# Optimization experiments

Measured on AMD Instinct MI355X. Metric: run time of the kernel, lower is better.

Reference implementation:

```python
import jax, jax.numpy as jnp
import numpy as np

B, IN, H = 256, 128, 512


def setup_inputs() -> dict:
    key = jax.random.key(0)
    ks = jax.random.split(key, 12)
    w = lambda k, shape: jax.random.normal(k, shape, dtype=jnp.float32) * 0.05
    return {
        "inputs": jax.random.normal(ks[0], (B, IN), dtype=jnp.float32),
        "h": jax.random.normal(ks[1], (B, H), dtype=jnp.float32),
        "c": jax.random.normal(ks[2], (B, H), dtype=jnp.float32),
        "ts": jax.random.uniform(ks[3], (B,), dtype=jnp.float32),
        # LSTMCell params (PyTorch layout: [4H, in], gate order i,f,g,o)
        "W_ih": w(ks[4], (4 * H, IN)),
        "W_hh": w(ks[5], (4 * H, H)),
        "b_ih": w(ks[6], (4 * H,)),
        "b_hh": w(ks[7], (4 * H,)),
        # ODE vector field: Linear(H,H) -> tanh -> Linear(H,H)
        "W1": w(ks[8], (H, H)),
        "b1": w(ks[9], (H,)),
        "W2": w(ks[10], (H, H)),
        "b2": w(ks[11], (H,)),
    }


def reference(inputs, h, c, ts, W_ih, W_hh, b_ih, b_hh, W1, b1, W2, b2):
    # --- LSTMCell ---
    gates = inputs @ W_ih.T + b_ih + h @ W_hh.T + b_hh  # [B, 4H]
    i_g, f_g, g_g, o_g = jnp.split(gates, 4, axis=-1)
    new_c = jax.nn.sigmoid(f_g) * c + jax.nn.sigmoid(i_g) * jnp.tanh(g_g)
    h0 = jax.nn.sigmoid(o_g) * jnp.tanh(new_c)  # [B, H]

    # --- sorted time grid ---
    bsz = ts.shape[0]
    indices = jnp.argsort(ts)
    s_sort = ts[indices] + jnp.linspace(0.0, 1e-4, bsz)  # strictly increasing

    # --- autonomous ODE vector field ---
    def f_ode(x):
        return jnp.tanh(x @ W1.T + b1) @ W2.T + b2

    # --- fixed-step RK4 trajectory at the sorted time points ---
    dts = s_sort[1:] - s_sort[:-1]  # [B-1]

    def step(hcur, dt):
        k1 = f_ode(hcur)
        k2 = f_ode(hcur + 0.5 * dt * k1)
        k3 = f_ode(hcur + 0.5 * dt * k2)
        k4 = f_ode(hcur + dt * k3)
        hn = hcur + (dt / 6.0) * (k1 + 2.0 * k2 + 2.0 * k3 + k4)
        return hn, hn

    _, traj_rest = jax.lax.scan(step, h0, dts)          # [B-1, B, H]
    traj = jnp.concatenate([h0[None], traj_rest], 0)    # [B, B, H]

    # per-batch-row time slice (faithful to trajectory[indices, arange(B)])
    new_h = traj[indices, jnp.arange(bsz)]  # [B, H]
    return new_h, new_c
```

## Files before the change

### kernel.cpp

```cpp
#include <hip/hip_runtime.h>

#define BB   256
#define IND  128
#define HD   512
#define KST  1
#define XSTR 648

typedef _Float16 f16x8 __attribute__((ext_vector_type(8)));
typedef float    f32x4 __attribute__((ext_vector_type(4)));

__device__ __forceinline__ float sigm(float x){ return 1.0f/(1.0f+__expf(-x)); }
__device__ __forceinline__ float tanhfast(float x){
  float e2 = __expf(2.0f*x);
  return 1.0f - 2.0f/(e2+1.0f);
}
__device__ __forceinline__ f16x8 cvt8(const float* s){
  f16x8 r;
  #pragma unroll
  for (int j=0;j<8;j++) r[j] = (_Float16)s[j];
  return r;
}

__device__ __forceinline__ f32x4 mv16(const _Float16* __restrict__ Ab,
    const f16x8* __restrict__ Bp, int m, int g){
  f16x8 af[16], bw[16];
  #pragma unroll
  for (int kt=0;kt<16;kt++)
    af[kt] = *(const f16x8*)&Ab[m*HD + kt*32 + 8*g];
  #pragma unroll
  for (int kt=0;kt<16;kt++)
    bw[kt] = Bp[kt*64];
  f32x4 acc = {0.f,0.f,0.f,0.f};
  #pragma unroll
  for (int kt=0;kt<16;kt++)
    acc = __builtin_amdgcn_mfma_f32_16x16x32_f16(af[kt], bw[kt], acc, 0,0,0);
  return acc;
}

__device__ __forceinline__ void packg_body(int b, int t,
    const float* __restrict__ Wih, const float* __restrict__ Whh,
    _Float16* __restrict__ Wgp){
  const int tile = b*4 + (t>>6);
  const int l = t & 63, m = l & 15, g = l >> 4;
  const int NT = tile/20, kt = tile - NT*20;
  const int n  = NT*16 + m;
  const int k0 = kt*32 + 8*g;
  const float* src = (kt < 4) ? (Wih + n*IND + k0) : (Whh + n*HD + (k0 - IND));
  *((f16x8*)(Wgp + tile*512) + l) = cvt8(src);
}

__device__ __forceinline__ void sort_body(int t, const float* __restrict__ ts,
    float* __restrict__ tau){
  __shared__ float sts[BB];
  __shared__ float ssort[BB];
  __shared__ int   sidx[BB];
  sts[t] = ts[t];
  __syncthreads();
  const float v = sts[t];
  int r = 0;
  for (int k=0;k<BB;k++){
    const float u = sts[k];
    r += (u < v) || (u == v && k < t);
  }
  ssort[r] = v + (float)r*(1e-4f/255.0f);
  sidx[r]  = t;
  __syncthreads();
  tau[t] = ssort[sidx[t]] - ssort[0];
}

__device__ __forceinline__ void packw_body(int tile, int t,
    const float* __restrict__ W, _Float16* __restrict__ Wp){
  const int l = t & 63, m = l & 15, g = l >> 4;
  const int NT = tile >> 4, kt = tile & 15;
  const float* src = W + (NT*16 + m)*HD + kt*32 + 8*g;
  *((f16x8*)(Wp + tile*512) + l) = cvt8(src);
}

__device__ __forceinline__ void packT_body(int unit, int t,
    const float* __restrict__ W2, _Float16* __restrict__ W2T){
  const int l = t & 63;
  const int kb = unit >> 5, jb = unit & 31;
  const int k0 = kb*64, j0 = jb*16;
  _Float16 v[16];
  #pragma unroll
  for (int i=0;i<16;i++)
    v[i] = (_Float16)W2[(j0+i)*HD + k0 + l];
  *(f16x8*)&W2T[(k0+l)*HD + j0]     = *(const f16x8*)&v[0];
  *(f16x8*)&W2T[(k0+l)*HD + j0 + 8] = *(const f16x8*)&v[8];
}

__device__ __forceinline__ void cvec_body(int n,
    const float* __restrict__ W1, const float* __restrict__ b2,
    float* __restrict__ cvec){
  float s = 0.f;
  for (int j=0;j<HD;j+=4){
    const float4 a = *(const float4*)(W1 + n*HD + j);
    const float4 bb = *(const float4*)(b2 + j);
    s += a.x*bb.x + a.y*bb.y + a.z*bb.z + a.w*bb.w;
  }
  cvec[n] = s;
}

__device__ __forceinline__ void gates_body(int b, int t,
    const float* __restrict__ inp, const float* __restrict__ h,
    const float* __restrict__ c,   const _Float16* __restrict__ Wgp,
    const float* __restrict__ bih, const float* __restrict__ bhh,
    _Float16* __restrict__ V, float* __restrict__ newc){
  __shared__ _Float16 X16[16*XSTR];
  __shared__ float    Gx[4][2][16][16];
  const int l = t & 63;
  const int w = t >> 6;
  const int m = l & 15;
  const int g = l >> 4;
  const int rt = b & 15;
  const int cq = b >> 4;
  const int r0 = rt * 16;

  for (int i=0;i<40;i++){
    const int e  = t + 256*i;
    const int rr = e / 640;
    const int k  = e - rr*640;
    const float v = (k < IND) ? inp[(r0+rr)*IND + k] : h[(r0+rr)*HD + (k-IND)];
    X16[rr*XSTR + k] = (_Float16)v;
  }
  __syncthreads();

  f16x8 af[20];
  #pragma unroll
  for (int kt=0;kt<20;kt++)
    af[kt] = *(const f16x8*)&X16[m*XSTR + kt*32 + 8*g];

  #pragma unroll
  for (int ht=0;ht<2;ht++){
    const int NT = w*32 + cq*2 + ht;
    const f16x8* bp = (const f16x8*)Wgp + (size_t)NT*20*64 + l;
    f16x8 bw[20];
    #pragma unroll
    for (int kt=0;kt<20;kt++) bw[kt] = bp[kt*64];
    f32x4 acc = {0.f,0.f,0.f,0.f};
    #pragma unroll
    for (int kt=0;kt<20;kt++)
      acc = __builtin_amdgcn_mfma_f32_16x16x32_f16(af[kt], bw[kt], acc, 0,0,0);
    #pragma unroll
    for (int r=0;r<4;r++) Gx[w][ht][4*g+r][m] = acc[r];
  }
  __syncthreads();

  #pragma unroll
  for (int p=0;p<2;p++){
    const int e   = t + 256*p;
    const int row = e >> 5;
    const int col = e & 31;
    const int ht  = col >> 4, mm = col & 15;
    const int hi  = cq*32 + col;
    const int grow = r0 + row;
    const float iv = Gx[0][ht][row][mm] + bih[hi]        + bhh[hi];
    const float fv = Gx[1][ht][row][mm] + bih[HD+hi]     + bhh[HD+hi];
    const float gv = Gx[2][ht][row][mm] + bih[2*HD+hi]   + bhh[2*HD+hi];
    const float ov = Gx[3][ht][row][mm] + bih[3*HD+hi]   + bhh[3*HD+hi];
    const float cv = c[grow*HD + hi];
    const float nc = sigm(fv)*cv + sigm(iv)*tanhfast(gv);
    const float hv = sigm(ov)*tanhfast(nc);
    newc[grow*HD + hi] = nc;
    V[grow*HD + hi]    = (_Float16)hv;
  }
}

__device__ __forceinline__ void mm_body(int tile, int t, int nw,
    const _Float16* __restrict__ W2T, const _Float16* __restrict__ W1p,
    _Float16* __restrict__ Mp){
  __shared__ float Mt[4][32][16];
  const int l = t & 63, w = t >> 6, m = l & 15, g = l >> 4;
  const int NT = tile >> 4, kt = tile & 15;
  const f16x8* bp = (const f16x8*)W1p + NT*16*64 + l;
  const f32x4 d0 = mv16(W2T + (kt*32     )*HD, bp, m, g);
  const f32x4 d1 = mv16(W2T + (kt*32 + 16)*HD, bp, m, g);
  #pragma unroll
  for (int r=0;r<4;r++){
    Mt[w][4*g+r][m]    = d0[r];
    Mt[w][16+4*g+r][m] = d1[r];
  }
  __syncthreads();
  _Float16 v[8];
  #pragma unroll
  for (int j=0;j<8;j++) v[j] = (_Float16)Mt[w][8*g+j][m];
  *((f16x8*)(Mp + tile*512) + l) = *(const f16x8*)v;
  (void)nw;
}

__device__ __forceinline__ void init0_body(int rb, int t,
    const _Float16* __restrict__ V, const _Float16* __restrict__ W1p,
    const float* __restrict__ b1, float* __restrict__ UB,
    _Float16* __restrict__ Y0, _Float16* __restrict__ YS0){
  const int l = t & 63, w = t >> 6, m = l & 15, g = l >> 4;
  const int rg = rb >> 4, cg = rb & 15;
  const int NT = cg*2 + w, cc = NT*16 + m;
  const f32x4 a = mv16(V + rg*16*HD, (const f16x8*)W1p + NT*16*64 + l, m, g);
  const float bv = b1[cc];
  #pragma unroll
  for (int r=0;r<4;r++){
    const int idx = (rg*16 + 4*g + r)*HD + cc;
    UB[idx] = a[r];
    const float y = tanhfast(a[r] + bv);
    Y0[idx]  = (_Float16)y;
    YS0[idx] = (_Float16)y;
  }
}


__global__ __launch_bounds__(256) void k_prep(
    const float* __restrict__ Wih, const float* __restrict__ Whh,
    const float* __restrict__ ts,  const float* __restrict__ W1,
    const float* __restrict__ W2,  const float* __restrict__ b2,
    _Float16* __restrict__ Wgp, float* __restrict__ tau,
    _Float16* __restrict__ W1p, _Float16* __restrict__ W2p,
    _Float16* __restrict__ W2T, float* __restrict__ cvec){
  const int b = blockIdx.x, t = threadIdx.x;
  if      (b < 640) packg_body(b, t, Wih, Whh, Wgp);
  else if (b == 640) sort_body(t, ts, tau);
  else if (b < 769) packw_body((b-641)*4 + (t>>6), t, W1, W1p);
  else if (b < 897) packw_body((b-769)*4 + (t>>6), t, W2, W2p);
  else if (b < 961) packT_body((b-897)*4 + (t>>6), t, W2, W2T);
  else              cvec_body((b-961)*256 + t, W1, b2, cvec);
}

__global__ __launch_bounds__(256) void k_prep1(
    const float* __restrict__ Wih, const float* __restrict__ Whh,
    const float* __restrict__ ts,  _Float16* __restrict__ Wgp,
    float* __restrict__ tau){
  const int b = blockIdx.x, t = threadIdx.x;
  if (b < 640) packg_body(b, t, Wih, Whh, Wgp);
  else         sort_body(t, ts, tau);
}
__global__ __launch_bounds__(256) void k_prep2(
    const float* __restrict__ W1, const float* __restrict__ W2,
    const float* __restrict__ b2, _Float16* __restrict__ W1p,
    _Float16* __restrict__ W2p, _Float16* __restrict__ W2T,
    float* __restrict__ cvec){
  const int b = blockIdx.x, t = threadIdx.x;
  if      (b < 128) packw_body(b*4 + (t>>6), t, W1, W1p);
  else if (b < 256) packw_body((b-128)*4 + (t>>6), t, W2, W2p);
  else if (b < 320) packT_body((b-256)*4 + (t>>6), t, W2, W2T);
  else              cvec_body((b-320)*256 + t, W1, b2, cvec);
}

__global__ __launch_bounds__(256) void k_gmm(
    const float* __restrict__ inp, const float* __restrict__ h,
    const float* __restrict__ c,   const _Float16* __restrict__ Wgp,
    const float* __restrict__ bih, const float* __restrict__ bhh,
    const _Float16* __restrict__ W2T, const _Float16* __restrict__ W1p,
    _Float16* __restrict__ V, float* __restrict__ newc,
    _Float16* __restrict__ Mp){
  const int b = blockIdx.x, t = threadIdx.x;
  if (b < 256) gates_body(b, t, inp, h, c, Wgp, bih, bhh, V, newc);
  else         mm_body((b-256)*4 + (t>>6), t, 4, W2T, W1p, Mp);
}

__global__ __launch_bounds__(256) void k_gates(
    const float* __restrict__ inp, const float* __restrict__ h,
    const float* __restrict__ c,   const _Float16* __restrict__ Wgp,
    const float* __restrict__ bih, const float* __restrict__ bhh,
    _Float16* __restrict__ V, float* __restrict__ newc){
  gates_body(blockIdx.x, threadIdx.x, inp, h, c, Wgp, bih, bhh, V, newc);
}

__global__ __launch_bounds__(128) void k_init0(
    const _Float16* __restrict__ V, const _Float16* __restrict__ W1p,
    const float* __restrict__ b1, float* __restrict__ UB,
    _Float16* __restrict__ Y0, _Float16* __restrict__ YS0){
  init0_body(blockIdx.x, threadIdx.x, V, W1p, b1, UB, Y0, YS0);
}

__global__ __launch_bounds__(128) void k_mi(
    const _Float16* __restrict__ W2T, const _Float16* __restrict__ W1p,
    const _Float16* __restrict__ V,   const float* __restrict__ b1,
    _Float16* __restrict__ Mp, float* __restrict__ UB,
    _Float16* __restrict__ Y0, _Float16* __restrict__ YS0){
  const int b = blockIdx.x, t = threadIdx.x;
  if (b < 256) mm_body(b*2 + (t>>6), t, 2, W2T, W1p, Mp);
  else         init0_body(b - 256, t, V, W1p, b1, UB, Y0, YS0);
}

__global__ __launch_bounds__(128) void k_stage(
    const _Float16* __restrict__ Yin, const _Float16* __restrict__ Mp,
    const float* __restrict__ cvec, const float* __restrict__ b1,
    const float* __restrict__ tau, const float* __restrict__ UB,
    _Float16* __restrict__ YS, _Float16* __restrict__ Yout, int st){
  const int t = threadIdx.x, l = t & 63, w = t >> 6, m = l & 15, g = l >> 4;
  const int rg = blockIdx.x >> 4, cg = blockIdx.x & 15;
  const int NT = cg*2 + w, cc = NT*16 + m;
  const f32x4 a = mv16(Yin + rg*16*HD, (const f16x8*)Mp + NT*16*64 + l, m, g);
  const float cv = cvec[cc];
  const float bv = b1[cc];
  const float wgt = (st==2) ? 1.f : 2.f;
  #pragma unroll
  for (int r=0;r<4;r++){
    const int row = rg*16 + 4*g + r;
    const int idx = row*HD + cc;
    const float dt = tau[row] * (1.0f/(float)KST);
    const float alpha = (st==2) ? dt : 0.5f*dt;
    const float u = UB[idx] + alpha*(a[r] + cv);
    const float y = tanhfast(u + bv);
    Yout[idx] = (_Float16)y;
    YS[idx]   = (_Float16)((float)YS[idx] + wgt*y);
  }
}

__global__ __launch_bounds__(128) void k_final1(
    const _Float16* __restrict__ YS, const _Float16* __restrict__ W2p,
    const float* __restrict__ b2, const float* __restrict__ tau,
    const _Float16* __restrict__ V, float* __restrict__ newh){
  const int t = threadIdx.x, l = t & 63, w = t >> 6, m = l & 15, g = l >> 4;
  const int rg = blockIdx.x >> 4, cg = blockIdx.x & 15;
  const int NT = cg*2 + w, cc = NT*16 + m;
  const _Float16 d6m = (_Float16)(tau[rg*16 + m] * (1.0f/(6.0f*(float)KST)));
  const f16x8* Bp = (const f16x8*)W2p + NT*16*64 + l;
  f16x8 af[16], bw[16];
  #pragma unroll
  for (int kt=0;kt<16;kt++){
    const f16x8 ay = *(const f16x8*)&YS[(rg*16 + m)*HD + kt*32 + 8*g];
    af[kt] = ay * d6m;
  }
  #pragma unroll
  for (int kt=0;kt<16;kt++) bw[kt] = Bp[kt*64];
  f32x4 a = {0.f,0.f,0.f,0.f};
  #pragma unroll
  for (int kt=0;kt<16;kt++)
    a = __builtin_amdgcn_mfma_f32_16x16x32_f16(af[kt], bw[kt], a, 0,0,0);
  const float bv = b2[cc];
  #pragma unroll
  for (int r=0;r<4;r++){
    const int row = rg*16 + 4*g + r;
    const int idx = row*HD + cc;
    newh[idx] = (float)V[idx] + a[r] + tau[row]*bv;
  }
}

extern "C" void kernel_launch(void* const* d_in, const int* in_sizes, int n_in,
                              void* d_out, int out_size, void* d_ws, size_t ws_size,
                              hipStream_t stream){
  const float* inp = (const float*)d_in[0];
  const float* h   = (const float*)d_in[1];
  const float* c   = (const float*)d_in[2];
  const float* ts  = (const float*)d_in[3];
  const float* Wih = (const float*)d_in[4];
  const float* Whh = (const float*)d_in[5];
  const float* bih = (const float*)d_in[6];
  const float* bhh = (const float*)d_in[7];
  const float* W1  = (const float*)d_in[8];
  const float* b1  = (const float*)d_in[9];
  const float* W2  = (const float*)d_in[10];
  const float* b2  = (const float*)d_in[11];

  float* newh = (float*)d_out;
  float* newc = (float*)d_out + BB*HD;

  char* base = (char*)d_ws;
  float*    tau  = (float*)base;
  float*    cvec = (float*)(base + 1024);
  _Float16* V    = (_Float16*)(base + 3072);
  float*    UB   = (float*)(base + 3072 + 262144);
  _Float16* Y0   = (_Float16*)(base + 3072 + 786432);
  _Float16* YS0  = (_Float16*)(base + 3072 + 1048576);
  _Float16* Y1   = (_Float16*)(base + 3072 + 1310720);
  char*     ov   = base + 3072 + 1572864;
  _Float16* W1p  = (_Float16*)ov;
  _Float16* W2p  = (_Float16*)(ov + 524288);
  _Float16* W2T  = (_Float16*)(ov + 1048576);
  _Float16* Mp   = (_Float16*)(ov + 1572864);
  const size_t NEED_FUSED = (size_t)(3072 + 1572864 + 2097152 + 2621440);

  if (ws_size >= NEED_FUSED){
    _Float16* Wgp = (_Float16*)(ov + 2097152);
    k_prep <<<963, 256, 0, stream>>>(Wih, Whh, ts, W1, W2, b2,
                                     Wgp, tau, W1p, W2p, W2T, cvec);
    k_gmm  <<<384, 256, 0, stream>>>(inp,h,c,Wgp,bih,bhh,W2T,W1p,V,newc,Mp);
    k_init0<<<256, 128, 0, stream>>>(V, W1p, b1, UB, Y0, YS0);
  } else {
    _Float16* Wgp = (_Float16*)ov;
    k_prep1<<<641, 256, 0, stream>>>(Wih, Whh, ts, Wgp, tau);
    k_gates<<<256, 256, 0, stream>>>(inp,h,c,Wgp,bih,bhh,V,newc);
    k_prep2<<<322, 256, 0, stream>>>(W1, W2, b2, W1p, W2p, W2T, cvec);
    k_mi   <<<512, 128, 0, stream>>>(W2T, W1p, V, b1, Mp, UB, Y0, YS0);
  }

  k_stage <<<256,128,0,stream>>>(Y0, Mp, cvec, b1, tau, UB, YS0, Y1, 0);
  k_stage <<<256,128,0,stream>>>(Y1, Mp, cvec, b1, tau, UB, YS0, Y0, 1);
  k_stage <<<256,128,0,stream>>>(Y0, Mp, cvec, b1, tau, UB, YS0, Y1, 2);
  k_final1<<<256,128,0,stream>>>(YS0, W2p, b2, tau, V, newh);
}
```

Measured before the change: 51.91 us.

## Stage A-operand rows in LDS and rebalance prep work across kernels

```diff
diff --git a/kernel.cpp b/kernel.cpp
--- a/kernel.cpp
+++ b/kernel.cpp
@@ -5,6 +5,7 @@
 #define HD   512
 #define KST  1
 #define XSTR 648
+#define VSTR 520
 
 typedef _Float16 f16x8 __attribute__((ext_vector_type(8)));
 typedef float    f32x4 __attribute__((ext_vector_type(4)));
@@ -35,6 +36,33 @@
   for (int kt=0;kt<16;kt++)
     acc = __builtin_amdgcn_mfma_f32_16x16x32_f16(af[kt], bw[kt], acc, 0,0,0);
   return acc;
+}
+
+__device__ __forceinline__ f32x4 mv16l(const _Float16* __restrict__ As,
+    const f16x8* __restrict__ Bp, int m, int g){
+  f16x8 af[16], bw[16];
+  #pragma unroll
+  for (int kt=0;kt<16;kt++)
+    af[kt] = *(const f16x8*)&As[m*VSTR + kt*32 + 8*g];
+  #pragma unroll
+  for (int kt=0;kt<16;kt++)
+    bw[kt] = Bp[kt*64];
+  f32x4 acc = {0.f,0.f,0.f,0.f};
+  #pragma unroll
+  for (int kt=0;kt<16;kt++)
+    acc = __builtin_amdgcn_mfma_f32_16x16x32_f16(af[kt], bw[kt], acc, 0,0,0);
+  return acc;
+}
+
+__device__ __forceinline__ void stage_A(int t, const _Float16* __restrict__ src,
+                                        _Float16* __restrict__ As){
+  const f16x8* s = (const f16x8*)src;
+  #pragma unroll
+  for (int i=0;i<8;i++){
+    const int u = t + 128*i;
+    const int row = u >> 6, c8 = u & 63;
+    *(f16x8*)&As[row*VSTR + c8*8] = s[u];
+  }
 }
 
 __device__ __forceinline__ void packg_body(int b, int t,
@@ -166,7 +194,7 @@
   }
 }
 
-__device__ __forceinline__ void mm_body(int tile, int t, int nw,
+__device__ __forceinline__ void mm_body(int tile, int t,
     const _Float16* __restrict__ W2T, const _Float16* __restrict__ W1p,
     _Float16* __restrict__ Mp){
   __shared__ float Mt[4][32][16];
@@ -185,7 +213,6 @@
   #pragma unroll
   for (int j=0;j<8;j++) v[j] = (_Float16)Mt[w][8*g+j][m];
   *((f16x8*)(Mp + tile*512) + l) = *(const f16x8*)v;
-  (void)nw;
 }
 
 __device__ __forceinline__ void init0_body(int rb, int t,
@@ -210,18 +237,31 @@
 
 __global__ __launch_bounds__(256) void k_prep(
     const float* __restrict__ Wih, const float* __restrict__ Whh,
-    const float* __restrict__ ts,  const float* __restrict__ W1,
-    const float* __restrict__ W2,  const float* __restrict__ b2,
-    _Float16* __restrict__ Wgp, float* __restrict__ tau,
-    _Float16* __restrict__ W1p, _Float16* __restrict__ W2p,
-    _Float16* __restrict__ W2T, float* __restrict__ cvec){
+    const float* __restrict__ W1,  const float* __restrict__ W2,
+    _Float16* __restrict__ Wgp, _Float16* __restrict__ W1p,
+    _Float16* __restrict__ W2T){
   const int b = blockIdx.x, t = threadIdx.x;
   if      (b < 640) packg_body(b, t, Wih, Whh, Wgp);
-  else if (b == 640) sort_body(t, ts, tau);
-  else if (b < 769) packw_body((b-641)*4 + (t>>6), t, W1, W1p);
-  else if (b < 897) packw_body((b-769)*4 + (t>>6), t, W2, W2p);
-  else if (b < 961) packT_body((b-897)*4 + (t>>6), t, W2, W2T);
-  else              cvec_body((b-961)*256 + t, W1, b2, cvec);
+  else if (b < 768) packw_body((b-640)*4 + (t>>6), t, W1, W1p);
+  else              packT_body((b-768)*4 + (t>>6), t, W2, W2T);
+}
+
+__global__ __launch_bounds__(256) void k_gmm(
+    const float* __restrict__ inp, const float* __restrict__ h,
+    const float* __restrict__ c,   const _Float16* __restrict__ Wgp,
+    const float* __restrict__ bih, const float* __restrict__ bhh,
+    const _Float16* __restrict__ W2T, const _Float16* __restrict__ W1p,
+    const float* __restrict__ W1, const float* __restrict__ W2,
+    const float* __restrict__ b2, const float* __restrict__ ts,
+    _Float16* __restrict__ V, float* __restrict__ newc,
+    _Float16* __restrict__ Mp, _Float16* __restrict__ W2p,
+    float* __restrict__ tau, float* __restrict__ cvec){
+  const int b = blockIdx.x, t = threadIdx.x;
+  if      (b < 256) gates_body(b, t, inp, h, c, Wgp, bih, bhh, V, newc);
+  else if (b < 384) mm_body((b-256)*4 + (t>>6), t, W2T, W1p, Mp);
+  else if (b < 512) packw_body((b-384)*4 + (t>>6), t, W2, W2p);
+  else if (b == 512) sort_body(t, ts, tau);
+  else              cvec_body((b-513)*256 + t, W1, b2, cvec);
 }
 
 __global__ __launch_bounds__(256) void k_prep1(
@@ -243,19 +283,6 @@
   else if (b < 320) packT_body((b-256)*4 + (t>>6), t, W2, W2T);
   else              cvec_body((b-320)*256 + t, W1, b2, cvec);
 }
-
-__global__ __launch_bounds__(256) void k_gmm(
-    const float* __restrict__ inp, const float* __restrict__ h,
-    const float* __restrict__ c,   const _Float16* __restrict__ Wgp,
-    const float* __restrict__ bih, const float* __restrict__ bhh,
-    const _Float16* __restrict__ W2T, const _Float16* __restrict__ W1p,
-    _Float16* __restrict__ V, float* __restrict__ newc,
-    _Float16* __restrict__ Mp){
-  const int b = blockIdx.x, t = threadIdx.x;
-  if (b < 256) gates_body(b, t, inp, h, c, Wgp, bih, bhh, V, newc);
-  else         mm_body((b-256)*4 + (t>>6), t, 4, W2T, W1p, Mp);
-}
-
 __global__ __launch_bounds__(256) void k_gates(
     const float* __restrict__ inp, const float* __restrict__ h,
     const float* __restrict__ c,   const _Float16* __restrict__ Wgp,
@@ -263,22 +290,39 @@
     _Float16* __restrict__ V, float* __restrict__ newc){
   gates_body(blockIdx.x, threadIdx.x, inp, h, c, Wgp, bih, bhh, V, newc);
 }
-
-__global__ __launch_bounds__(128) void k_init0(
-    const _Float16* __restrict__ V, const _Float16* __restrict__ W1p,
-    const float* __restrict__ b1, float* __restrict__ UB,
-    _Float16* __restrict__ Y0, _Float16* __restrict__ YS0){
-  init0_body(blockIdx.x, threadIdx.x, V, W1p, b1, UB, Y0, YS0);
-}
-
 __global__ __launch_bounds__(128) void k_mi(
     const _Float16* __restrict__ W2T, const _Float16* __restrict__ W1p,
     const _Float16* __restrict__ V,   const float* __restrict__ b1,
     _Float16* __restrict__ Mp, float* __restrict__ UB,
     _Float16* __restrict__ Y0, _Float16* __restrict__ YS0){
   const int b = blockIdx.x, t = threadIdx.x;
-  if (b < 256) mm_body(b*2 + (t>>6), t, 2, W2T, W1p, Mp);
-  else         init0_body(b - 256, t, V, W1p, b1, UB, Y0, YS0);
+  if (b < 256){
+    mm_body(b*2 + (t>>6), t, W2T, W1p, Mp);
+  } else {
+    init0_body(b - 256, t, V, W1p, b1, UB, Y0, YS0);
+  }
+}
+
+__global__ __launch_bounds__(128) void k_init0(
+    const _Float16* __restrict__ V, const _Float16* __restrict__ W1p,
+    const float* __restrict__ b1, float* __restrict__ UB,
+    _Float16* __restrict__ Y0, _Float16* __restrict__ YS0){
+  __shared__ _Float16 As[16*VSTR];
+  const int t = threadIdx.x, l = t & 63, w = t >> 6, m = l & 15, g = l >> 4;
+  const int rg = blockIdx.x >> 4, cg = blockIdx.x & 15;
+  stage_A(t, V + rg*16*HD, As);
+  __syncthreads();
+  const int NT = cg*2 + w, cc = NT*16 + m;
+  const f32x4 a = mv16l(As, (const f16x8*)W1p + NT*16*64 + l, m, g);
+  const float bv = b1[cc];
+  #pragma unroll
+  for (int r=0;r<4;r++){
+    const int idx = (rg*16 + 4*g + r)*HD + cc;
+    UB[idx] = a[r];
+    const float y = tanhfast(a[r] + bv);
+    Y0[idx]  = (_Float16)y;
+    YS0[idx] = (_Float16)y;
+  }
 }
 
 __global__ __launch_bounds__(128) void k_stage(
@@ -286,10 +330,13 @@
     const float* __restrict__ cvec, const float* __restrict__ b1,
     const float* __restrict__ tau, const float* __restrict__ UB,
     _Float16* __restrict__ YS, _Float16* __restrict__ Yout, int st){
+  __shared__ _Float16 As[16*VSTR];
   const int t = threadIdx.x, l = t & 63, w = t >> 6, m = l & 15, g = l >> 4;
   const int rg = blockIdx.x >> 4, cg = blockIdx.x & 15;
+  stage_A(t, Yin + rg*16*HD, As);
+  __syncthreads();
   const int NT = cg*2 + w, cc = NT*16 + m;
-  const f32x4 a = mv16(Yin + rg*16*HD, (const f16x8*)Mp + NT*16*64 + l, m, g);
+  const f32x4 a = mv16l(As, (const f16x8*)Mp + NT*16*64 + l, m, g);
   const float cv = cvec[cc];
   const float bv = b1[cc];
   const float wgt = (st==2) ? 1.f : 2.f;
@@ -310,15 +357,18 @@
     const _Float16* __restrict__ YS, const _Float16* __restrict__ W2p,
     const float* __restrict__ b2, const float* __restrict__ tau,
     const _Float16* __restrict__ V, float* __restrict__ newh){
+  __shared__ _Float16 As[16*VSTR];
   const int t = threadIdx.x, l = t & 63, w = t >> 6, m = l & 15, g = l >> 4;
   const int rg = blockIdx.x >> 4, cg = blockIdx.x & 15;
+  stage_A(t, YS + rg*16*HD, As);
+  __syncthreads();
   const int NT = cg*2 + w, cc = NT*16 + m;
   const _Float16 d6m = (_Float16)(tau[rg*16 + m] * (1.0f/(6.0f*(float)KST)));
   const f16x8* Bp = (const f16x8*)W2p + NT*16*64 + l;
   f16x8 af[16], bw[16];
   #pragma unroll
   for (int kt=0;kt<16;kt++){
-    const f16x8 ay = *(const f16x8*)&YS[(rg*16 + m)*HD + kt*32 + 8*g];
+    const f16x8 ay = *(const f16x8*)&As[m*VSTR + kt*32 + 8*g];
     af[kt] = ay * d6m;
   }
   #pragma unroll
@@ -372,9 +422,9 @@
 
   if (ws_size >= NEED_FUSED){
     _Float16* Wgp = (_Float16*)(ov + 2097152);
-    k_prep <<<963, 256, 0, stream>>>(Wih, Whh, ts, W1, W2, b2,
-                                     Wgp, tau, W1p, W2p, W2T, cvec);
-    k_gmm  <<<384, 256, 0, stream>>>(inp,h,c,Wgp,bih,bhh,W2T,W1p,V,newc,Mp);
+    k_prep <<<832, 256, 0, stream>>>(Wih, Whh, W1, W2, Wgp, W1p, W2T);
+    k_gmm  <<<515, 256, 0, stream>>>(inp,h,c,Wgp,bih,bhh,W2T,W1p,W1,W2,b2,ts,
+                                     V,newc,Mp,W2p,tau,cvec);
     k_init0<<<256, 128, 0, stream>>>(V, W1p, b1, UB, Y0, YS0);
   } else {
     _Float16* Wgp = (_Float16*)ov;
```

Result: faster. 49.10 us (-5.4%).
